# Kernel tuning notes

Hardware: AMD Instinct MI355X
Metric: run time of the kernel (lower is better)

## Reference

```python
import jax, jax.numpy as jnp
import numpy as np
from jax import lax

B, T, I, H, O = 64, 512, 256, 1024, 1


def setup_inputs() -> dict:
    key = jax.random.key(0)
    ks = jax.random.split(key, 7)
    s_ih = 1.0 / np.sqrt(H)
    return {
        "x": jax.random.normal(ks[0], (B, T, I), dtype=jnp.float32),
        "W_ih": jax.random.uniform(ks[1], (4 * H, I), minval=-s_ih, maxval=s_ih, dtype=jnp.float32),
        "W_hh": jax.random.uniform(ks[2], (4 * H, H), minval=-s_ih, maxval=s_ih, dtype=jnp.float32),
        "b_ih": jax.random.uniform(ks[3], (4 * H,), minval=-s_ih, maxval=s_ih, dtype=jnp.float32),
        "b_hh": jax.random.uniform(ks[4], (4 * H,), minval=-s_ih, maxval=s_ih, dtype=jnp.float32),
        "fc_W": jax.random.uniform(ks[5], (O, H), minval=-s_ih, maxval=s_ih, dtype=jnp.float32),
        "fc_b": jax.random.uniform(ks[6], (O,), minval=-s_ih, maxval=s_ih, dtype=jnp.float32),
    }


def reference(x, W_ih, W_hh, b_ih, b_hh, fc_W, fc_b):
    Bd, Td, _ = x.shape
    Hd = W_hh.shape[1]
    # Precompute input projections for all timesteps: [T, B, 4H]
    x_proj = jnp.einsum('bti,gi->tbg', x, W_ih) + b_ih + b_hh

    def step(carry, xt):
        h, c = carry
        gates = xt + h @ W_hh.T  # [B, 4H]
        i_g, f_g, g_g, o_g = jnp.split(gates, 4, axis=-1)  # PyTorch order i,f,g,o
        i_g = jax.nn.sigmoid(i_g)
        f_g = jax.nn.sigmoid(f_g)
        g_g = jnp.tanh(g_g)
        o_g = jax.nn.sigmoid(o_g)
        c_new = f_g * c + i_g * g_g
        h_new = o_g * jnp.tanh(c_new)
        return (h_new, c_new), None

    h0 = jnp.zeros((Bd, Hd), dtype=x.dtype)
    c0 = jnp.zeros((Bd, Hd), dtype=x.dtype)
    (h_last, _), _ = lax.scan(step, (h0, c0), x_proj)
    out = jnp.tanh(h_last)          # tanh on last hidden state
    return out @ fc_W.T + fc_b      # [B, O]
```

## Files before the change

kernel.cpp:

```cpp
#include <hip/hip_runtime.h>
#include <hip/hip_bf16.h>


typedef __bf16 bf16_t;
typedef bf16_t b16x8 __attribute__((ext_vector_type(8)));
typedef float  f32x4 __attribute__((ext_vector_type(4)));
typedef unsigned u32x4 __attribute__((ext_vector_type(4)));

#define TQ 512
#define IQ 256
#define HQ 1024

union U8 { b16x8 b; unsigned long long q[2]; unsigned short u[8]; };
union HU { f32x4 f; b16x8 b; };

__device__ __forceinline__ float bf2f(unsigned short s) {
    return __uint_as_float(((unsigned)s) << 16);
}
__device__ __forceinline__ unsigned short f2bf(float f) {
    unsigned u = __float_as_uint(f);
    u += 0x7fff + ((u >> 16) & 1);
    return (unsigned short)(u >> 16);
}
__device__ __forceinline__ b16x8 cvt84(float4 a, float4 b) {
    U8 r;
    r.u[0] = f2bf(a.x); r.u[1] = f2bf(a.y); r.u[2] = f2bf(a.z); r.u[3] = f2bf(a.w);
    r.u[4] = f2bf(b.x); r.u[5] = f2bf(b.y); r.u[6] = f2bf(b.z); r.u[7] = f2bf(b.w);
    return r.b;
}
__device__ __forceinline__ float frcp(float x) { return __builtin_amdgcn_rcpf(x); }
__device__ __forceinline__ float sigm(float x) { return frcp(1.f + __expf(-x)); }
__device__ __forceinline__ float tanh_f(float v) {
    float x = fminf(fmaxf(v, -15.f), 15.f);
    float e = __expf(2.f * x);
    return (e - 1.f) * frcp(e + 1.f);
}

__device__ __forceinline__ unsigned ld_flag_sys(const unsigned* p) {
    unsigned v;
    asm volatile("global_load_dword %0, %1, off sc0 sc1\n\ts_waitcnt vmcnt(0)"
                 : "=v"(v) : "v"(p) : "memory");
    return v;
}
__device__ __forceinline__ void st_flag_sys(unsigned* p, unsigned v) {
    asm volatile("global_store_dword %0, %1, off sc0 sc1" :: "v"(p), "v"(v) : "memory");
}
__device__ __forceinline__ void st_h16_sys(unsigned short* p, unsigned short v) {
    asm volatile("global_store_short %0, %1, off sc0 sc1" :: "v"(p), "v"(v) : "memory");
}
__device__ __forceinline__ void ld_h4(b16x8* ah, const unsigned short* p) {
    HU a, b, c, d;
    asm volatile(
        "global_load_dwordx4 %0, %4, off sc0 sc1\n\t"
        "global_load_dwordx4 %1, %4, off offset:64 sc0 sc1\n\t"
        "global_load_dwordx4 %2, %4, off offset:128 sc0 sc1\n\t"
        "global_load_dwordx4 %3, %4, off offset:192 sc0 sc1\n\t"
        "s_waitcnt vmcnt(0)"
        : "=&v"(a.f), "=&v"(b.f), "=&v"(c.f), "=&v"(d.f) : "v"(p) : "memory");
    ah[0] = a.b; ah[1] = b.b; ah[2] = c.b; ah[3] = d.b;
}
__device__ __forceinline__ void ld_h2_dev(b16x8* ah, const unsigned short* p) {
    HU a, b;
    asm volatile(
        "global_load_dwordx4 %0, %2, off sc0 sc1\n\t"
        "global_load_dwordx4 %1, %2, off offset:16 sc0 sc1\n\t"
        "s_waitcnt vmcnt(0)"
        : "=&v"(a.f), "=&v"(b.f) : "v"(p) : "memory");
    ah[0] = a.b; ah[1] = b.b;
}
__device__ __forceinline__ u32x4 ld_flag4_dev(const unsigned* p) {
    u32x4 v;
    asm volatile("global_load_dwordx4 %0, %1, off sc0 sc1\n\ts_waitcnt vmcnt(0)"
                 : "=v"(v) : "v"(p) : "memory");
    return v;
}

#define A_HCOPY_SH 131072
#define A_HBG_SH   16384
#define A_HPBUF_SH 8192
#define A_BCOPY_W  8192
#define A_OFF_FH    524288
#define A_OFF_BAR   655360
#define A_OFF_FBAR  720896
#define MEMSET_BYTES 753664
#define RED2(ww,g,u,b) (((((ww)*4 + (g))*16 + (u))*12) + (b))

__launch_bounds__(256, 2)
__global__ void lstm_a(const float* __restrict__ x,
                       const float* __restrict__ Wih,
                       const float* __restrict__ Whh,
                       const float* __restrict__ bih,
                       const float* __restrict__ bhh,
                       const float* __restrict__ fcW,
                       const float* __restrict__ fcb,
                       float* __restrict__ out,
                       char* __restrict__ ws)
{
    __shared__ float red[4 * 4 * 16 * 12];

    unsigned short* hb   = (unsigned short*)ws;
    unsigned short* fh   = (unsigned short*)(ws + A_OFF_FH);
    unsigned*       bar  = (unsigned*)(ws + A_OFF_BAR);
    unsigned*       fbar = (unsigned*)(ws + A_OFF_FBAR);

    const int tid  = threadIdx.x;
    const int w    = tid >> 6;
    const int lane = tid & 63;
    const int bid  = blockIdx.x;
    const int bg   = bid & 7;
    const int ug   = bid >> 3;
    const int par  = ug & 1;

    const int l16  = lane & 15;
    const int quad = lane >> 4;

    b16x8 wih[2][4];
    b16x8 whh[8][4];
    {
        const int koff = quad * 8;
        #pragma unroll
        for (int g = 0; g < 4; ++g) {
            int row = g * HQ + ug * 16 + l16;
            #pragma unroll
            for (int c = 0; c < 2; ++c) {
                const float* p = Wih + (size_t)row * IQ + w * 64 + c * 32 + koff;
                wih[c][g] = cvt84(*(const float4*)p, *(const float4*)(p + 4));
            }
            #pragma unroll
            for (int j = 0; j < 8; ++j) {
                const float* q = Whh + (size_t)row * HQ + w * 256 + j * 32 + koff;
                whh[j][g] = cvt84(*(const float4*)q, *(const float4*)(q + 4));
            }
        }
    }

    const int hi  = (lane >> 5) & 1;
    const int eb  = 2 * w + hi;
    const int dup = (lane >> 4) & 1;
    float c_st = 0.f, h_last = 0.f;
    float bias_g[4];
    #pragma unroll
    for (int g = 0; g < 4; ++g) {
        int gr = g * HQ + ug * 16 + l16;
        bias_g[g] = bih[gr] + bhh[gr];
    }

    const unsigned short* hrd0 = hb + (size_t)par * A_HCOPY_SH + (size_t)bg * A_HBG_SH
                               + (size_t)(l16 & 7) * 1024 + w * 256 + quad * 8;
    unsigned short* hwr0 = hb + (size_t)bg * A_HBG_SH + (size_t)eb * 1024 + ug * 16 + l16;
    const unsigned* myfl = bar + (size_t)par * A_BCOPY_W
                         + ((size_t)(bg * 64 + w * 16 + (lane >> 2)) * 16 + (lane & 3));
    unsigned* wfl0 = bar + ((size_t)(bg * 64 + ug) * 16 + w);
    unsigned* wfl1 = wfl0 + A_BCOPY_W;

    const float* xbase = x + ((size_t)(bg * 8 + (l16 & 7)) * TQ) * IQ + w * 64 + quad * 8;
    float4 xa = *(const float4*)(xbase);
    float4 xb = *(const float4*)(xbase + 4);
    float4 xc = *(const float4*)(xbase + 32);
    float4 xd = *(const float4*)(xbase + 36);

    for (int t = 0; t < TQ; ++t) {
        const int p = t & 1;

        b16x8 ax0 = cvt84(xa, xb);
        b16x8 ax1 = cvt84(xc, xd);
        f32x4 acc[4];
        #pragma unroll
        for (int g = 0; g < 4; ++g) {
            f32x4 z = {0.f, 0.f, 0.f, 0.f};
            acc[g] = __builtin_amdgcn_mfma_f32_16x16x32_bf16(ax0, wih[0][g], z, 0, 0, 0);
            acc[g] = __builtin_amdgcn_mfma_f32_16x16x32_bf16(ax1, wih[1][g], acc[g], 0, 0, 0);
        }

        if (t) {
            const unsigned need = (unsigned)t;
            unsigned v = ld_flag_sys(myfl);
            while (!__all(v >= need)) v = ld_flag_sys(myfl);

            const unsigned short* hp = hrd0 + (size_t)p * A_HPBUF_SH;
            b16x8 ah[4];
            ld_h4(ah, hp);
            #pragma unroll
            for (int j = 0; j < 4; ++j) {
                #pragma unroll
                for (int g = 0; g < 4; ++g)
                    acc[g] = __builtin_amdgcn_mfma_f32_16x16x32_bf16(ah[j], whh[j][g], acc[g], 0, 0, 0);
            }
            ld_h4(ah, hp + 128);
            #pragma unroll
            for (int j = 0; j < 4; ++j) {
                #pragma unroll
                for (int g = 0; g < 4; ++g)
                    acc[g] = __builtin_amdgcn_mfma_f32_16x16x32_bf16(ah[j], whh[4 + j][g], acc[g], 0, 0, 0);
            }
        }

        __syncthreads();
        if (quad < 2) {
            #pragma unroll
            for (int g = 0; g < 4; ++g)
                *(f32x4*)&red[RED2(w, g, l16, quad * 4)] = acc[g];
        }
        __syncthreads();

        float s[4];
        #pragma unroll
        for (int g = 0; g < 4; ++g) {
            float a0 = red[RED2(dup * 2 + 0, g, l16, eb)]
                     + red[RED2(dup * 2 + 1, g, l16, eb)];
            s[g] = a0 + __shfl_xor(a0, 16);
        }
        {
            float gi = s[0] + bias_g[0];
            float gf = s[1] + bias_g[1];
            float gg = s[2] + bias_g[2];
            float go_ = s[3] + bias_g[3];
            float i_s = sigm(gi);
            float f_s = sigm(gf);
            float g_t = tanh_f(gg);
            float o_s = sigm(go_);
            float c = f_s * c_st + i_s * g_t;
            c_st = c;
            float h = o_s * tanh_f(c);
            h_last = h;
            if (!dup) {
                unsigned short hv = f2bf(h);
                st_h16_sys(hwr0 + (size_t)(p ^ 1) * A_HPBUF_SH, hv);
                st_h16_sys(hwr0 + A_HCOPY_SH + (size_t)(p ^ 1) * A_HPBUF_SH, hv);
            }
        }
        asm volatile("s_waitcnt vmcnt(0)" ::: "memory");
        if (lane == 0) {
            st_flag_sys(wfl0, (unsigned)(t + 1));
            st_flag_sys(wfl1, (unsigned)(t + 1));
        }

        size_t nt = (t + 1 < TQ) ? (size_t)(t + 1) * IQ : (size_t)t * IQ;
        xa = *(const float4*)(xbase + nt);
        xb = *(const float4*)(xbase + nt + 4);
        xc = *(const float4*)(xbase + nt + 32);
        xd = *(const float4*)(xbase + nt + 36);
    }

    if (!dup)
        st_h16_sys(fh + ((size_t)(bg * 8 + eb)) * 1024 + ug * 16 + l16, f2bf(h_last));
    asm volatile("s_waitcnt vmcnt(0)" ::: "memory");
    if (lane == 0) st_flag_sys(fbar + ((size_t)(bg * 64 + ug) * 16 + w), 1u);

    if (ug == 0) {
        const unsigned* pf = fbar + ((size_t)(bg * 64 + lane) * 16);
        for (;;) {
            u32x4 v = ld_flag4_dev(pf);
            if (__all(v[0] == 1u && v[1] == 1u && v[2] == 1u && v[3] == 1u)) break;
        }
        float fb = fcb[0];
        #pragma unroll
        for (int r = 0; r < 2; ++r) {
            int b = w * 2 + r;
            b16x8 hv[2];
            ld_h2_dev(hv, fh + ((size_t)(bg * 8 + b)) * 1024 + lane * 16);
            float sacc = 0.f;
            #pragma unroll
            for (int k = 0; k < 2; ++k) {
                U8 u; u.b = hv[k];
                #pragma unroll
                for (int e = 0; e < 8; ++e)
                    sacc += tanh_f(bf2f(u.u[e])) * fcW[lane * 16 + k * 8 + e];
            }
            #pragma unroll
            for (int off = 32; off > 0; off >>= 1)
                sacc += __shfl_down(sacc, off);
            if (lane == 0) out[bg * 8 + b] = sacc + fb;
        }
    }
}

#define RED_B(w,g,u,b) (((((w)*4 + (g))*16 + (u))*20) + (b))
#define B_HCOPY 131072
#define B_HPBUF 65536
#define B_BCOPY 4096

__launch_bounds__(512, 2)
__global__ void lstm_b(const float* __restrict__ x,
                       const float* __restrict__ Wih,
                       const float* __restrict__ Whh,
                       const float* __restrict__ bih,
                       const float* __restrict__ bhh,
                       const float* __restrict__ fcW,
                       const float* __restrict__ fcb,
                       float* __restrict__ out,
                       unsigned short* __restrict__ hbuf,
                       unsigned int* __restrict__ bar)
{
    __shared__ float red[8 * 4 * 16 * 20];

    const int tid  = threadIdx.x;
    const int w    = tid >> 6;
    const int lane = tid & 63;
    const int bid  = blockIdx.x;
    const int bg   = bid & 3;
    const int ug   = bid >> 2;
    const int par  = ug & 1;

    const int l16  = lane & 15;
    const int quad = lane >> 4;

    b16x8 wih[4];
    b16x8 whh[4][4];
    {
        const int koff = quad * 8;
        #pragma unroll
        for (int g = 0; g < 4; ++g) {
            int row = g * HQ + ug * 16 + l16;
            const float* p = Wih + (size_t)row * IQ + w * 32 + koff;
            float4 a = *(const float4*)p;
            float4 b = *(const float4*)(p + 4);
            wih[g] = cvt84(a, b);
            #pragma unroll
            for (int j = 0; j < 4; ++j) {
                int k0 = (w * 4 + j) * 32 + koff;
                const float* q = Whh + (size_t)row * HQ + k0;
                float4 c = *(const float4*)q;
                float4 e = *(const float4*)(q + 4);
                whh[j][g] = cvt84(c, e);
            }
        }
    }

    const int hi  = (lane >> 5) & 1;
    const int eb  = 2 * w + hi;
    const int dup = (lane >> 4) & 1;
    float c_st = 0.f;
    float bias_g[4];
    #pragma unroll
    for (int g = 0; g < 4; ++g) {
        int gr = g * HQ + ug * 16 + l16;
        bias_g[g] = bih[gr] + bhh[gr];
    }

    const unsigned short* hrd0 = hbuf + (size_t)par * B_HCOPY
                               + ((size_t)bg * 16 + l16) * HQ + w * 128 + quad * 8;
    unsigned short* hwr0 = hbuf + (size_t)bg * 16 * HQ + (size_t)eb * HQ + ug * 16 + l16;

    const unsigned int* myfl = bar + (size_t)par * B_BCOPY
                             + ((size_t)(bg * 64 + w * 8 + (lane >> 3)) * 16 + (lane & 7));
    unsigned int* wfl0 = bar + ((size_t)(bg * 64 + ug) * 16 + w);
    unsigned int* wfl1 = wfl0 + B_BCOPY;

    const float* xbase = x + ((size_t)(bg * 16 + l16) * TQ) * IQ + w * 32 + quad * 8;
    float4 xa = *(const float4*)(xbase);
    float4 xb = *(const float4*)(xbase + 4);

    for (int t = 0; t < TQ; ++t) {
        const int p = t & 1;

        b16x8 ax = cvt84(xa, xb);
        f32x4 acc[4];
        #pragma unroll
        for (int g = 0; g < 4; ++g) {
            f32x4 z = {0.f, 0.f, 0.f, 0.f};
            acc[g] = __builtin_amdgcn_mfma_f32_16x16x32_bf16(ax, wih[g], z, 0, 0, 0);
        }

        const unsigned need = (unsigned)t;
        {
            unsigned v = __hip_atomic_load(myfl, __ATOMIC_RELAXED,
                                           __HIP_MEMORY_SCOPE_AGENT);
            while (!__all(v >= need))
                v = __hip_atomic_load(myfl, __ATOMIC_RELAXED,
                                      __HIP_MEMORY_SCOPE_AGENT);
        }

        b16x8 ah[4];
        ld_h4(ah, hrd0 + (size_t)p * B_HPBUF);
        #pragma unroll
        for (int j = 0; j < 4; ++j) {
            #pragma unroll
            for (int g = 0; g < 4; ++g)
                acc[g] = __builtin_amdgcn_mfma_f32_16x16x32_bf16(ah[j], whh[j][g], acc[g], 0, 0, 0);
        }

        __syncthreads();
        #pragma unroll
        for (int g = 0; g < 4; ++g)
            *(f32x4*)&red[RED_B(w, g, l16, quad * 4)] = acc[g];
        __syncthreads();

        float s[4];
        #pragma unroll
        for (int g = 0; g < 4; ++g) {
            float a0 = red[RED_B(dup * 4 + 0, g, l16, eb)]
                     + red[RED_B(dup * 4 + 1, g, l16, eb)];
            float a1 = red[RED_B(dup * 4 + 2, g, l16, eb)]
                     + red[RED_B(dup * 4 + 3, g, l16, eb)];
            float as = a0 + a1;
            as += __shfl_xor(as, 16);
            s[g] = as;
        }
        {
            float gi = s[0] + bias_g[0];
            float gf = s[1] + bias_g[1];
            float gg = s[2] + bias_g[2];
            float go_ = s[3] + bias_g[3];
            float i_s = sigm(gi);
            float f_s = sigm(gf);
            float g_t = tanh_f(gg);
            float o_s = sigm(go_);
            float c = f_s * c_st + i_s * g_t;
            c_st = c;
            float h = o_s * tanh_f(c);
            if (!dup) {
                unsigned short hv = f2bf(h);
                __hip_atomic_store(hwr0 + (size_t)(p ^ 1) * B_HPBUF, hv,
                                   __ATOMIC_RELAXED, __HIP_MEMORY_SCOPE_AGENT);
                __hip_atomic_store(hwr0 + B_HCOPY + (size_t)(p ^ 1) * B_HPBUF, hv,
                                   __ATOMIC_RELAXED, __HIP_MEMORY_SCOPE_AGENT);
            }
        }
        asm volatile("s_waitcnt vmcnt(0)" ::: "memory");
        if (lane == 0) {
            __hip_atomic_store(wfl0, (unsigned)(t + 1),
                               __ATOMIC_RELAXED, __HIP_MEMORY_SCOPE_AGENT);
            __hip_atomic_store(wfl1, (unsigned)(t + 1),
                               __ATOMIC_RELAXED, __HIP_MEMORY_SCOPE_AGENT);
        }

        size_t nt = (t + 1 < TQ) ? (size_t)(t + 1) * IQ : (size_t)t * IQ;
        xa = *(const float4*)(xbase + nt);
        xb = *(const float4*)(xbase + nt + 4);
    }

    if (bid < 4) {
        #pragma unroll
        for (int pb = 0; pb < 8; ++pb) {
            const unsigned int* pf = bar + ((size_t)(bg * 64 + pb * 8 + (lane >> 3)) * 16 + (lane & 7));
            unsigned v = __hip_atomic_load(pf, __ATOMIC_RELAXED,
                                           __HIP_MEMORY_SCOPE_AGENT);
            while (!__all(v >= (unsigned)TQ))
                v = __hip_atomic_load(pf, __ATOMIC_RELAXED,
                                      __HIP_MEMORY_SCOPE_AGENT);
        }
        const unsigned short* hl = hbuf + (size_t)bg * 16 * HQ;
        float fb = fcb[0];
        #pragma unroll
        for (int r = 0; r < 2; ++r) {
            int b = w * 2 + r;
            float sacc = 0.f;
            #pragma unroll
            for (int j = 0; j < 16; ++j) {
                int u = j * 64 + lane;
                unsigned short hv = __hip_atomic_load(hl + (size_t)b * HQ + u,
                                                      __ATOMIC_RELAXED,
                                                      __HIP_MEMORY_SCOPE_AGENT);
                sacc += tanh_f(bf2f(hv)) * fcW[u];
            }
            #pragma unroll
            for (int off = 32; off > 0; off >>= 1)
                sacc += __shfl_down(sacc, off);
            if (lane == 0) out[bg * 16 + b] = sacc + fb;
        }
    }
}

extern "C" void kernel_launch(void* const* d_in, const int* in_sizes, int n_in,
                              void* d_out, int out_size, void* d_ws, size_t ws_size,
                              hipStream_t stream) {
    (void)in_sizes; (void)n_in; (void)out_size; (void)ws_size;
    const float* x   = (const float*)d_in[0];
    const float* Wih = (const float*)d_in[1];
    const float* Whh = (const float*)d_in[2];
    const float* bih = (const float*)d_in[3];
    const float* bhh = (const float*)d_in[4];
    const float* fcW = (const float*)d_in[5];
    const float* fcb = (const float*)d_in[6];
    float* out = (float*)d_out;

    hipMemsetAsync(d_ws, 0, MEMSET_BYTES, stream);

    static int mode = -1;
    if (mode < 0) {
        int nb = 0;
        hipError_t e = hipOccupancyMaxActiveBlocksPerMultiprocessor(
            &nb, reinterpret_cast<const void*>(lstm_a), 256, 0);
        mode = (e == hipSuccess && nb >= 2) ? 1 : 0;
    }

    if (mode == 1) {
        char* ws = (char*)d_ws;
        void* args[] = { &x, &Wih, &Whh, &bih, &bhh, &fcW, &fcb, &out, &ws };
        hipError_t e = hipLaunchCooperativeKernel(
            reinterpret_cast<void*>(lstm_a), dim3(512), dim3(256), args, 0, stream);
        if (e == hipSuccess) return;
        mode = 0;
    }

    unsigned short* hbuf = (unsigned short*)d_ws;
    unsigned int*   bar  = (unsigned int*)((char*)d_ws + 524288);
    void* argsb[] = { &x, &Wih, &Whh, &bih, &bhh, &fcW, &fcb, &out, &hbuf, &bar };
    hipLaunchCooperativeKernel(reinterpret_cast<void*>(lstm_b),
                               dim3(256), dim3(512), argsb, 0, stream);
}
```

Before: 2.136 ms.

## Use XCD-local cache scope for recurrent exchange when block-to-XCD mapping matches

At kernel start each block reads its hardware XCC ID and checks whether it matches its batch-group index. Block 0 gathers these checks through a workspace control area and broadcasts a go word. If every block sits on the expected XCD, the per-step h-vector stores, loads and flag polling use sc0 only instead of sc0 sc1, which is meant to keep traffic in the local L2 rather than going to system coherence. Flags now carry an epoch tag so stale values from earlier launches are not mistaken for progress. The cost is a grid-wide startup handshake, and correctness depends on the runtime mapping block IDs to XCDs round-robin.

```diff
diff --git a/kernel.cpp b/kernel.cpp
--- a/kernel.cpp
+++ b/kernel.cpp
@@ -36,21 +36,32 @@
     return (e - 1.f) * frcp(e + 1.f);
 }
 
-__device__ __forceinline__ unsigned ld_flag_sys(const unsigned* p) {
+__device__ __forceinline__ unsigned ld_flag_f(const unsigned* p, bool fast) {
     unsigned v;
-    asm volatile("global_load_dword %0, %1, off sc0 sc1\n\ts_waitcnt vmcnt(0)"
-                 : "=v"(v) : "v"(p) : "memory");
+    if (fast) asm volatile("global_load_dword %0, %1, off sc0\n\ts_waitcnt vmcnt(0)"
+                           : "=v"(v) : "v"(p) : "memory");
+    else      asm volatile("global_load_dword %0, %1, off sc0 sc1\n\ts_waitcnt vmcnt(0)"
+                           : "=v"(v) : "v"(p) : "memory");
     return v;
 }
-__device__ __forceinline__ void st_flag_sys(unsigned* p, unsigned v) {
-    asm volatile("global_store_dword %0, %1, off sc0 sc1" :: "v"(p), "v"(v) : "memory");
-}
-__device__ __forceinline__ void st_h16_sys(unsigned short* p, unsigned short v) {
-    asm volatile("global_store_short %0, %1, off sc0 sc1" :: "v"(p), "v"(v) : "memory");
-}
-__device__ __forceinline__ void ld_h4(b16x8* ah, const unsigned short* p) {
+__device__ __forceinline__ void st_flag_f(unsigned* p, unsigned v, bool fast) {
+    if (fast) asm volatile("global_store_dword %0, %1, off sc0" :: "v"(p), "v"(v) : "memory");
+    else      asm volatile("global_store_dword %0, %1, off sc0 sc1" :: "v"(p), "v"(v) : "memory");
+}
+__device__ __forceinline__ void st_h16_f(unsigned short* p, unsigned short v, bool fast) {
+    if (fast) asm volatile("global_store_short %0, %1, off sc0" :: "v"(p), "v"(v) : "memory");
+    else      asm volatile("global_store_short %0, %1, off sc0 sc1" :: "v"(p), "v"(v) : "memory");
+}
+__device__ __forceinline__ void ld_h4_f(b16x8* ah, const unsigned short* p, bool fast) {
     HU a, b, c, d;
-    asm volatile(
+    if (fast) asm volatile(
+        "global_load_dwordx4 %0, %4, off sc0\n\t"
+        "global_load_dwordx4 %1, %4, off offset:64 sc0\n\t"
+        "global_load_dwordx4 %2, %4, off offset:128 sc0\n\t"
+        "global_load_dwordx4 %3, %4, off offset:192 sc0\n\t"
+        "s_waitcnt vmcnt(0)"
+        : "=&v"(a.f), "=&v"(b.f), "=&v"(c.f), "=&v"(d.f) : "v"(p) : "memory");
+    else asm volatile(
         "global_load_dwordx4 %0, %4, off sc0 sc1\n\t"
         "global_load_dwordx4 %1, %4, off offset:64 sc0 sc1\n\t"
         "global_load_dwordx4 %2, %4, off offset:128 sc0 sc1\n\t"
@@ -58,6 +69,15 @@
         "s_waitcnt vmcnt(0)"
         : "=&v"(a.f), "=&v"(b.f), "=&v"(c.f), "=&v"(d.f) : "v"(p) : "memory");
     ah[0] = a.b; ah[1] = b.b; ah[2] = c.b; ah[3] = d.b;
+}
+__device__ __forceinline__ void st_h16_sys(unsigned short* p, unsigned short v) {
+    asm volatile("global_store_short %0, %1, off sc0 sc1" :: "v"(p), "v"(v) : "memory");
+}
+__device__ __forceinline__ void st_flag_sys(unsigned* p, unsigned v) {
+    asm volatile("global_store_dword %0, %1, off sc0 sc1" :: "v"(p), "v"(v) : "memory");
+}
+__device__ __forceinline__ void ld_h4_sys(b16x8* ah, const unsigned short* p) {
+    ld_h4_f(ah, p, false);
 }
 __device__ __forceinline__ void ld_h2_dev(b16x8* ah, const unsigned short* p) {
     HU a, b;
@@ -82,7 +102,9 @@
 #define A_OFF_FH    524288
 #define A_OFF_BAR   655360
 #define A_OFF_FBAR  720896
-#define MEMSET_BYTES 753664
+#define A_OFF_CTRL  753664
+#define MEMSET_BYTES 753920
+#define A_OFF_EPOCH 753920
 #define RED2(ww,g,u,b) (((((ww)*4 + (g))*16 + (u))*12) + (b))
 
 __launch_bounds__(256, 2)
@@ -97,11 +119,14 @@
                        char* __restrict__ ws)
 {
     __shared__ float red[4 * 4 * 16 * 12];
-
-    unsigned short* hb   = (unsigned short*)ws;
-    unsigned short* fh   = (unsigned short*)(ws + A_OFF_FH);
-    unsigned*       bar  = (unsigned*)(ws + A_OFF_BAR);
-    unsigned*       fbar = (unsigned*)(ws + A_OFF_FBAR);
+    __shared__ unsigned bc[1];
+
+    unsigned short* hb    = (unsigned short*)ws;
+    unsigned short* fh    = (unsigned short*)(ws + A_OFF_FH);
+    unsigned*       bar   = (unsigned*)(ws + A_OFF_BAR);
+    unsigned*       fbar  = (unsigned*)(ws + A_OFF_FBAR);
+    unsigned*       ctl   = (unsigned*)(ws + A_OFF_CTRL);
+    unsigned*       epoch = (unsigned*)(ws + A_OFF_EPOCH);
 
     const int tid  = threadIdx.x;
     const int w    = tid >> 6;
@@ -114,6 +139,15 @@
     const int l16  = lane & 15;
     const int quad = lane >> 4;
 
+    if (tid == 0) {
+        unsigned xcd;
+        asm volatile("s_getreg_b32 %0, hwreg(HW_REG_XCC_ID)" : "=s"(xcd));
+        if ((int)(xcd & 7) != bg)
+            __hip_atomic_fetch_or(ctl + 4, 1u, __ATOMIC_RELAXED, __HIP_MEMORY_SCOPE_AGENT);
+        __threadfence();
+        __hip_atomic_fetch_add(ctl + 0, 1u, __ATOMIC_RELAXED, __HIP_MEMORY_SCOPE_AGENT);
+    }
+
     b16x8 wih[2][4];
     b16x8 whh[8][4];
     {
@@ -133,6 +167,31 @@
             }
         }
     }
+
+    if (tid == 0) {
+        unsigned g;
+        if (bid == 0) {
+            unsigned e = (__hip_atomic_fetch_add(epoch, 1u, __ATOMIC_RELAXED,
+                                                 __HIP_MEMORY_SCOPE_AGENT) + 1u) & 0xFFFFFu;
+            while (__hip_atomic_load(ctl + 0, __ATOMIC_RELAXED,
+                                     __HIP_MEMORY_SCOPE_AGENT) < 512u) {}
+            __threadfence();
+            unsigned m = __hip_atomic_load(ctl + 4, __ATOMIC_RELAXED,
+                                           __HIP_MEMORY_SCOPE_AGENT);
+            g = (e << 2) | (m ? 2u : 1u);
+            __hip_atomic_store(ctl + 8, g, __ATOMIC_RELAXED, __HIP_MEMORY_SCOPE_AGENT);
+        } else {
+            do {
+                g = __hip_atomic_load(ctl + 8, __ATOMIC_RELAXED,
+                                      __HIP_MEMORY_SCOPE_AGENT);
+            } while (!g);
+        }
+        bc[0] = g;
+    }
+    __syncthreads();
+    const unsigned go   = bc[0];
+    const bool     fast = (go & 3u) == 1u;
+    const unsigned etag = go >> 2;
 
     const int hi  = (lane >> 5) & 1;
     const int eb  = 2 * w + hi;
@@ -173,20 +232,20 @@
         }
 
         if (t) {
-            const unsigned need = (unsigned)t;
-            unsigned v = ld_flag_sys(myfl);
-            while (!__all(v >= need)) v = ld_flag_sys(myfl);
+            unsigned v = ld_flag_f(myfl, fast);
+            while (!__all(((v >> 11) == etag) & ((v & 0x7FFu) >= (unsigned)t)))
+                v = ld_flag_f(myfl, fast);
 
             const unsigned short* hp = hrd0 + (size_t)p * A_HPBUF_SH;
             b16x8 ah[4];
-            ld_h4(ah, hp);
+            ld_h4_f(ah, hp, fast);
             #pragma unroll
             for (int j = 0; j < 4; ++j) {
                 #pragma unroll
                 for (int g = 0; g < 4; ++g)
                     acc[g] = __builtin_amdgcn_mfma_f32_16x16x32_bf16(ah[j], whh[j][g], acc[g], 0, 0, 0);
             }
-            ld_h4(ah, hp + 128);
+            ld_h4_f(ah, hp + 128, fast);
             #pragma unroll
             for (int j = 0; j < 4; ++j) {
                 #pragma unroll
@@ -225,14 +284,15 @@
             h_last = h;
             if (!dup) {
                 unsigned short hv = f2bf(h);
-                st_h16_sys(hwr0 + (size_t)(p ^ 1) * A_HPBUF_SH, hv);
-                st_h16_sys(hwr0 + A_HCOPY_SH + (size_t)(p ^ 1) * A_HPBUF_SH, hv);
+                st_h16_f(hwr0 + (size_t)(p ^ 1) * A_HPBUF_SH, hv, fast);
+                st_h16_f(hwr0 + A_HCOPY_SH + (size_t)(p ^ 1) * A_HPBUF_SH, hv, fast);
             }
         }
         asm volatile("s_waitcnt vmcnt(0)" ::: "memory");
         if (lane == 0) {
-            st_flag_sys(wfl0, (unsigned)(t + 1));
-            st_flag_sys(wfl1, (unsigned)(t + 1));
+            unsigned fv = (etag << 11) | (unsigned)(t + 1);
+            st_flag_f(wfl0, fv, fast);
+            st_flag_f(wfl1, fv, fast);
         }
 
         size_t nt = (t + 1 < TQ) ? (size_t)(t + 1) * IQ : (size_t)t * IQ;
@@ -372,7 +432,7 @@
         }
 
         b16x8 ah[4];
-        ld_h4(ah, hrd0 + (size_t)p * B_HPBUF);
+        ld_h4_sys(ah, hrd0 + (size_t)p * B_HPBUF);
         #pragma unroll
         for (int j = 0; j < 4; ++j) {
             #pragma unroll
```

New measurement: 2.097 ms. Within noise of the previous version (-1.8%).
